# Optimization experiments

Hardware: AMD Instinct MI355X
Metric: run time of the kernel (lower is better)

## Reference

```python
import jax, jax.numpy as jnp
import numpy as np

NEG_BIG = -1e9

def setup_inputs() -> dict:
    key = jax.random.key(0)
    kq, kk, kv, kwq, kwk, kwv, km = jax.random.split(key, 7)
    B, S, d = 16, 1024, 512
    Q = jax.random.normal(kq, (B, S, d), dtype=jnp.float32)
    K = jax.random.normal(kk, (B, S, d), dtype=jnp.float32)
    V = jax.random.normal(kv, (B, S, d), dtype=jnp.float32)
    # nn.Linear weights [d, d]; torch applies x @ W.T
    WQ = jax.random.normal(kwq, (d, d), dtype=jnp.float32) / np.sqrt(d)
    WK = jax.random.normal(kwk, (d, d), dtype=jnp.float32) / np.sqrt(d)
    WV = jax.random.normal(kwv, (d, d), dtype=jnp.float32) / np.sqrt(d)
    mask = jax.random.randint(km, (B, S), 0, 2, dtype=jnp.int32)
    return {"Q": Q, "K": K, "V": V, "WQ": WQ, "WK": WK, "WV": WV, "mask": mask}


def reference(Q, K, V, WQ, WK, WV, mask):
    d = Q.shape[-1]
    q = jnp.einsum('bsd,ed->bse', Q, WQ)
    k = jnp.einsum('bsd,ed->bse', K, WK)
    v = jnp.einsum('bsd,ed->bse', V, WV)
    scores = jnp.einsum('bqd,bkd->bqk', q, k) / jnp.sqrt(jnp.float32(d))
    attn = jax.nn.softmax(scores, axis=-1)
    # Faithful to original: mask applied AFTER softmax with -1e9 fill
    m = mask[:, None, :]  # [B,1,S] broadcast over query dim
    attn = jnp.where(m == 0, jnp.float32(NEG_BIG), attn)
    out = jnp.einsum('bqk,bkd->bqd', attn, v)
    return (out, attn)
```

## Files before the change

kernel.cpp:

```cpp
#include <hip/hip_runtime.h>
#include <hip/hip_bf16.h>

typedef float f32x4 __attribute__((ext_vector_type(4)));
typedef __bf16 bf16x8 __attribute__((ext_vector_type(8)));
typedef unsigned short u16x8 __attribute__((ext_vector_type(8)));
typedef int i32x4 __attribute__((ext_vector_type(4)));

#define NEG_BIG_F (-1000000000.0f)
#define SCALE_F 0.044194173824159216f

__device__ __forceinline__ unsigned short f2bf(float f) {
  unsigned int u = __float_as_uint(f);
  u += 0x7FFFu + ((u >> 16) & 1u);
  return (unsigned short)(u >> 16);
}

__device__ __forceinline__ float bf2f(unsigned short h) {
  return __uint_as_float((unsigned int)h << 16);
}

__device__ __forceinline__ u16x8 cvt8(f32x4 a, f32x4 b) {
  u16x8 r;
  r[0] = f2bf(a[0]); r[1] = f2bf(a[1]); r[2] = f2bf(a[2]); r[3] = f2bf(a[3]);
  r[4] = f2bf(b[0]); r[5] = f2bf(b[1]); r[6] = f2bf(b[2]); r[7] = f2bf(b[3]);
  return r;
}

__device__ __forceinline__ void gload16(const void* g, char* l) {
  __builtin_amdgcn_global_load_lds(
      (const __attribute__((address_space(1))) unsigned int*)g,
      (__attribute__((address_space(3))) unsigned int*)l, 16, 0, 0);
}

__global__ __launch_bounds__(256) void cvtW(
    const float* __restrict__ w0, const float* __restrict__ w1,
    const float* __restrict__ w2, unsigned short* __restrict__ out)
{
  const float* src = blockIdx.z == 0 ? w0 : (blockIdx.z == 1 ? w1 : w2);
  unsigned short* dst = out + (size_t)blockIdx.z * 262144;
  const int i = (blockIdx.x * 256 + threadIdx.x) * 8;
  f32x4 a = *(const f32x4*)(src + i);
  f32x4 b = *(const f32x4*)(src + i + 4);
  *(u16x8*)&dst[i] = cvt8(a, b);
}

__global__ __launch_bounds__(512, 2) void proj_all(
    const float* __restrict__ Q, const float* __restrict__ Kx,
    const float* __restrict__ V, const unsigned short* __restrict__ wb,
    unsigned short* __restrict__ qb, unsigned short* __restrict__ kb,
    unsigned short* __restrict__ vt)
{
  __shared__ __align__(16) unsigned short lds[32768];

  const int bid = blockIdx.x;
  const int tid = threadIdx.x;
  const int lane = tid & 63, wave = tid >> 6;
  const int fr = lane & 15, fq = lane >> 4;

  if (bid < 256) {
    const int z = bid >> 7, rem = bid & 127;
    const float* X = z ? Kx : Q;
    const unsigned short* W = wb + (size_t)z * 262144;
    unsigned short* Y = z ? kb : qb;
    const int m0 = (rem & 63) * 256, n0 = (rem >> 6) * 256;
    const int wr = (wave >> 2) * 128, wc = (wave & 3) * 64;

    unsigned short (*As)[256][32] = (unsigned short (*)[256][32])lds;
    unsigned short (*Bs)[256][32] = (unsigned short (*)[256][32])(lds + 16384);

    f32x4 acc[8][4] = {};

    int arow_s[2], aswz_s[2];
    const float* gAs[2];
    #pragma unroll
    for (int i = 0; i < 2; i++) {
      const int c = tid + 512 * i;
      arow_s[i] = c >> 2;
      aswz_s[i] = ((c & 3) ^ ((arow_s[i] >> 1) & 3)) * 8;
      gAs[i] = X + (size_t)(m0 + arow_s[i]) * 512 + (c & 3) * 8;
    }
    const unsigned short* gB[2]; char* lB[2];
    #pragma unroll
    for (int i = 0; i < 2; i++) {
      const int c = tid + 512 * i, row = c >> 2, slot = c & 3;
      gB[i] = W + (size_t)(n0 + row) * 512 + (slot ^ ((row >> 1) & 3)) * 8;
      lB[i] = (char*)(lds + 16384) + c * 16;
    }

    f32x4 pa[2][2];
    #pragma unroll
    for (int i = 0; i < 2; i++) {
      pa[i][0] = *(const f32x4*)(gAs[i]);
      pa[i][1] = *(const f32x4*)(gAs[i] + 4);
    }
    #pragma unroll
    for (int i = 0; i < 2; i++) gload16(gB[i], lB[i]);
    #pragma unroll
    for (int i = 0; i < 2; i++)
      *(u16x8*)&As[0][arow_s[i]][aswz_s[i]] = cvt8(pa[i][0], pa[i][1]);

    int cur = 0;
    for (int kt = 0; kt < 512; kt += 32) {
      const int nb = cur ^ 1;
      if (kt < 480) {
        #pragma unroll
        for (int i = 0; i < 2; i++) {
          pa[i][0] = *(const f32x4*)(gAs[i] + kt + 32);
          pa[i][1] = *(const f32x4*)(gAs[i] + kt + 36);
        }
        #pragma unroll
        for (int i = 0; i < 2; i++) gload16(gB[i] + kt + 32, lB[i] + nb * 16384);
        asm volatile("s_waitcnt vmcnt(6) lgkmcnt(0)" ::: "memory");
      } else {
        asm volatile("s_waitcnt vmcnt(0) lgkmcnt(0)" ::: "memory");
      }
      __builtin_amdgcn_sched_barrier(0);
      __builtin_amdgcn_s_barrier();

      bf16x8 bv[4];
      #pragma unroll
      for (int nf = 0; nf < 4; nf++) {
        const int br = wc + nf * 16 + fr;
        bv[nf] = *(const bf16x8*)&Bs[cur][br][(fq ^ ((br >> 1) & 3)) * 8];
      }
      #pragma unroll
      for (int mf = 0; mf < 8; mf++) {
        const int ar = wr + mf * 16 + fr;
        bf16x8 av = *(const bf16x8*)&As[cur][ar][(fq ^ ((ar >> 1) & 3)) * 8];
        #pragma unroll
        for (int nf = 0; nf < 4; nf++)
          acc[mf][nf] = __builtin_amdgcn_mfma_f32_16x16x32_bf16(av, bv[nf], acc[mf][nf], 0, 0, 0);
      }

      if (kt < 480) {
        #pragma unroll
        for (int i = 0; i < 2; i++)
          *(u16x8*)&As[nb][arow_s[i]][aswz_s[i]] = cvt8(pa[i][0], pa[i][1]);
      }
      __builtin_amdgcn_s_barrier();
      cur = nb;
    }

    #pragma unroll
    for (int mf = 0; mf < 8; mf++)
      #pragma unroll
      for (int nf = 0; nf < 4; nf++)
        #pragma unroll
        for (int rr = 0; rr < 4; rr++) {
          const int m = m0 + wr + mf * 16 + fq * 4 + rr;
          const int n = n0 + wc + nf * 16 + fr;
          Y[(size_t)m * 512 + n] = f2bf(acc[mf][nf][rr]);
        }
  } else {
    const int c0 = bid - 256;
    const int m0 = (c0 & 3) * 128, n0 = ((c0 >> 2) & 3) * 256, b = c0 >> 4;
    const int wr = (wave >> 2) * 64, wc = (wave & 3) * 64;
    const unsigned short* wv = wb + 524288;

    unsigned short (*As)[128][32] = (unsigned short (*)[128][32])lds;
    unsigned short (*Bs)[256][32] = (unsigned short (*)[256][32])(lds + 8192);

    f32x4 acc[4][4] = {};

    const int ar_s = tid >> 2, aslot = tid & 3;
    const unsigned short* gA = wv + (size_t)(m0 + ar_s) * 512 + (aslot ^ ((ar_s >> 1) & 3)) * 8;
    char* lA = (char*)lds + tid * 16;

    int brow_s[2], bswz_s[2];
    const float* gBs[2];
    #pragma unroll
    for (int i = 0; i < 2; i++) {
      const int c = tid + 512 * i;
      brow_s[i] = c >> 2;
      bswz_s[i] = ((c & 3) ^ ((brow_s[i] >> 1) & 3)) * 8;
      gBs[i] = V + ((size_t)b * 1024 + n0 + brow_s[i]) * 512 + (c & 3) * 8;
    }

    f32x4 pb[2][2];
    #pragma unroll
    for (int i = 0; i < 2; i++) {
      pb[i][0] = *(const f32x4*)(gBs[i]);
      pb[i][1] = *(const f32x4*)(gBs[i] + 4);
    }
    gload16(gA, lA);
    #pragma unroll
    for (int i = 0; i < 2; i++)
      *(u16x8*)&Bs[0][brow_s[i]][bswz_s[i]] = cvt8(pb[i][0], pb[i][1]);

    int cur = 0;
    for (int kt = 0; kt < 512; kt += 32) {
      const int nb = cur ^ 1;
      if (kt < 480) {
        #pragma unroll
        for (int i = 0; i < 2; i++) {
          pb[i][0] = *(const f32x4*)(gBs[i] + kt + 32);
          pb[i][1] = *(const f32x4*)(gBs[i] + kt + 36);
        }
        gload16(gA + kt + 32, lA + nb * 8192);
        asm volatile("s_waitcnt vmcnt(5) lgkmcnt(0)" ::: "memory");
      } else {
        asm volatile("s_waitcnt vmcnt(0) lgkmcnt(0)" ::: "memory");
      }
      __builtin_amdgcn_sched_barrier(0);
      __builtin_amdgcn_s_barrier();

      bf16x8 av[4], bv[4];
      #pragma unroll
      for (int mf = 0; mf < 4; mf++) {
        const int ar = wr + mf * 16 + fr;
        av[mf] = *(const bf16x8*)&As[cur][ar][(fq ^ ((ar >> 1) & 3)) * 8];
      }
      #pragma unroll
      for (int nf = 0; nf < 4; nf++) {
        const int br = wc + nf * 16 + fr;
        bv[nf] = *(const bf16x8*)&Bs[cur][br][(fq ^ ((br >> 1) & 3)) * 8];
      }
      #pragma unroll
      for (int mf = 0; mf < 4; mf++)
        #pragma unroll
        for (int nf = 0; nf < 4; nf++)
          acc[mf][nf] = __builtin_amdgcn_mfma_f32_16x16x32_bf16(av[mf], bv[nf], acc[mf][nf], 0, 0, 0);

      if (kt < 480) {
        #pragma unroll
        for (int i = 0; i < 2; i++)
          *(u16x8*)&Bs[nb][brow_s[i]][bswz_s[i]] = cvt8(pb[i][0], pb[i][1]);
      }
      __builtin_amdgcn_s_barrier();
      cur = nb;
    }

    #pragma unroll
    for (int mf = 0; mf < 4; mf++)
      #pragma unroll
      for (int nf = 0; nf < 4; nf++)
        #pragma unroll
        for (int rr = 0; rr < 4; rr++) {
          const int e = m0 + wr + mf * 16 + fq * 4 + rr;
          const int s = n0 + wc + nf * 16 + fr;
          vt[((size_t)b * 512 + e) * 1024 + s] = f2bf(acc[mf][nf][rr]);
        }
  }
}

__global__ __launch_bounds__(512, 2) void score256(
    const unsigned short* __restrict__ qb, const unsigned short* __restrict__ kb,
    const int* __restrict__ mask,
    unsigned short* __restrict__ P, float* __restrict__ partial)
{
  __shared__ __align__(16) unsigned short As[2][256][32];
  __shared__ __align__(16) unsigned short Bs[2][256][32];

  const int tid = threadIdx.x, bz = blockIdx.z;
  const int m0 = blockIdx.x * 256, n0 = blockIdx.y * 256;
  const int lane = tid & 63, wave = tid >> 6;
  const int wr = (wave >> 2) * 128, wc = (wave & 3) * 64;
  const int fr = lane & 15, fq = lane >> 4;

  f32x4 acc[8][4] = {};

  const unsigned short* gA[2]; char* lA[2];
  const unsigned short* gB[2]; char* lB[2];
  #pragma unroll
  for (int i = 0; i < 2; i++) {
    const int c = tid + 512 * i, row = c >> 2, slot = c & 3;
    const int sw = (slot ^ ((row >> 1) & 3)) * 8;
    gA[i] = qb + ((size_t)bz * 1024 + m0 + row) * 512 + sw;
    gB[i] = kb + ((size_t)bz * 1024 + n0 + row) * 512 + sw;
    lA[i] = (char*)&As[0][0][0] + c * 16;
    lB[i] = (char*)&Bs[0][0][0] + c * 16;
  }

  #pragma unroll
  for (int i = 0; i < 2; i++) { gload16(gA[i], lA[i]); gload16(gB[i], lB[i]); }

  int cur = 0;
  for (int kt = 0; kt < 512; kt += 32) {
    const int nb = cur ^ 1;
    if (kt < 480) {
      #pragma unroll
      for (int i = 0; i < 2; i++) {
        gload16(gA[i] + kt + 32, lA[i] + nb * 16384);
        gload16(gB[i] + kt + 32, lB[i] + nb * 16384);
      }
      asm volatile("s_waitcnt vmcnt(4) lgkmcnt(0)" ::: "memory");
    } else {
      asm volatile("s_waitcnt vmcnt(0) lgkmcnt(0)" ::: "memory");
    }
    __builtin_amdgcn_sched_barrier(0);
    __builtin_amdgcn_s_barrier();

    bf16x8 bv[4];
    #pragma unroll
    for (int nf = 0; nf < 4; nf++) {
      const int br = wc + nf * 16 + fr;
      bv[nf] = *(const bf16x8*)&Bs[cur][br][(fq ^ ((br >> 1) & 3)) * 8];
    }
    #pragma unroll
    for (int mf = 0; mf < 8; mf++) {
      const int ar = wr + mf * 16 + fr;
      bf16x8 av = *(const bf16x8*)&As[cur][ar][(fq ^ ((ar >> 1) & 3)) * 8];
      #pragma unroll
      for (int nf = 0; nf < 4; nf++)
        acc[mf][nf] = __builtin_amdgcn_mfma_f32_16x16x32_bf16(av, bv[nf], acc[mf][nf], 0, 0, 0);
    }
    __builtin_amdgcn_s_barrier();
    cur = nb;
  }

  int mcol[4];
  #pragma unroll
  for (int nf = 0; nf < 4; nf++)
    mcol[nf] = mask[bz * 1024 + n0 + wc + nf * 16 + fr];

  unsigned short* Pb = P + ((size_t)bz << 20);
  const int slot = blockIdx.y * 4 + (wave & 3);
  #pragma unroll
  for (int mf = 0; mf < 8; mf++) {
    #pragma unroll
    for (int rr = 0; rr < 4; rr++) {
      const int m = m0 + wr + mf * 16 + fq * 4 + rr;
      float e = 0.f;
      #pragma unroll
      for (int nf = 0; nf < 4; nf++) {
        const float ev = __expf(acc[mf][nf][rr] * SCALE_F);
        e += ev;
        Pb[(size_t)m * 1024 + n0 + wc + nf * 16 + fr] =
            mcol[nf] ? f2bf(ev) : (unsigned short)0;
      }
      e += __shfl_xor(e, 1); e += __shfl_xor(e, 2);
      e += __shfl_xor(e, 4); e += __shfl_xor(e, 8);
      if (fr == 0)
        partial[(size_t)slot * 16384 + bz * 1024 + m] = e;
    }
  }
}

__global__ __launch_bounds__(256) void mv_attn(
    const unsigned short* __restrict__ vt, const unsigned short* __restrict__ P,
    const float* __restrict__ partial, const int* __restrict__ mask,
    float* __restrict__ mvsum, float* __restrict__ attn)
{
  const int bid = blockIdx.x;
  const int tid = threadIdx.x;
  if (bid < 2048) {
    const int row = bid * 4 + (tid >> 6);
    const int b = row >> 9;
    const int lane = tid & 63;
    const unsigned short* vr = vt + (size_t)row * 1024 + lane * 16;
    const int* mr = mask + b * 1024 + lane * 16;
    u16x8 v0 = *(const u16x8*)(vr);
    u16x8 v1 = *(const u16x8*)(vr + 8);
    float s = 0.f;
    #pragma unroll
    for (int j = 0; j < 8; j++) {
      if (!mr[j])     s += bf2f(v0[j]);
      if (!mr[8 + j]) s += bf2f(v1[j]);
    }
    #pragma unroll
    for (int o = 32; o > 0; o >>= 1) s += __shfl_xor(s, o);
    if (lane == 0) mvsum[row] = s;
  } else {
    const int ab = bid - 2048;
    __shared__ float s_inv[2];
    const int row0 = ab * 2;
    if (tid < 2) {
      float s = 0.f;
      #pragma unroll
      for (int p = 0; p < 16; p++) s += partial[(size_t)p * 16384 + row0 + tid];
      s_inv[tid] = 1.0f / s;
    }
    __syncthreads();
    const size_t base = (size_t)ab * 2048 + tid * 8;
    const int b = (int)(base >> 20);
    const int k0 = (int)(base & 1023);
    const u16x8 p8 = *(const u16x8*)(P + base);
    const float iv = s_inv[tid >> 7];
    const int* mr = mask + b * 1024 + k0;
    const i32x4 ma = *(const i32x4*)(mr);
    const i32x4 mb = *(const i32x4*)(mr + 4);
    f32x4 o0, o1;
    o0[0] = ma[0] ? bf2f(p8[0]) * iv : NEG_BIG_F;
    o0[1] = ma[1] ? bf2f(p8[1]) * iv : NEG_BIG_F;
    o0[2] = ma[2] ? bf2f(p8[2]) * iv : NEG_BIG_F;
    o0[3] = ma[3] ? bf2f(p8[3]) * iv : NEG_BIG_F;
    o1[0] = mb[0] ? bf2f(p8[4]) * iv : NEG_BIG_F;
    o1[1] = mb[1] ? bf2f(p8[5]) * iv : NEG_BIG_F;
    o1[2] = mb[2] ? bf2f(p8[6]) * iv : NEG_BIG_F;
    o1[3] = mb[3] ? bf2f(p8[7]) * iv : NEG_BIG_F;
    *(f32x4*)(attn + base) = o0;
    *(f32x4*)(attn + base + 4) = o1;
  }
}

__global__ __launch_bounds__(512) void pv_gemm(
    const unsigned short* __restrict__ P, const unsigned short* __restrict__ vt,
    const float* __restrict__ partial, const float* __restrict__ mvsum,
    float* __restrict__ out)
{
  __shared__ __align__(16) unsigned short As[2][64][32];
  __shared__ __align__(16) unsigned short Bs[2][512][32];
  __shared__ float inv_l[64];

  const int tid = threadIdx.x;
  const int bz = blockIdx.z, m0 = blockIdx.x * 64;
  const int lane = tid & 63, wave = tid >> 6;
  const int n0 = wave * 64;
  const int fr = lane & 15, fq = lane >> 4;

  f32x4 acc[4][4] = {};

  if (tid < 64) {
    float s = 0.f;
    #pragma unroll
    for (int p = 0; p < 16; p++) s += partial[(size_t)p * 16384 + bz * 1024 + m0 + tid];
    inv_l[tid] = 1.0f / s;
  }

  const unsigned short* gA = nullptr; char* lA = nullptr;
  if (tid < 256) {
    const int row = tid >> 2, slot = tid & 3;
    gA = P + ((size_t)bz << 20) + (size_t)(m0 + row) * 1024 + (slot ^ ((row >> 1) & 3)) * 8;
    lA = (char*)&As[0][0][0] + tid * 16;
  }
  const unsigned short* gB[4]; char* lB[4];
  #pragma unroll
  for (int i = 0; i < 4; i++) {
    const int c = tid + 512 * i, row = c >> 2, slot = c & 3;
    gB[i] = vt + ((size_t)bz * 512 + row) * 1024 + (slot ^ ((row >> 1) & 3)) * 8;
    lB[i] = (char*)&Bs[0][0][0] + c * 16;
  }

  if (tid < 256) gload16(gA, lA);
  #pragma unroll
  for (int i = 0; i < 4; i++) gload16(gB[i], lB[i]);

  int cur = 0;
  for (int t = 0; t < 32; t++) {
    const int nb = cur ^ 1;
    const int kt = t * 32;
    if (t < 31) {
      if (tid < 256) gload16(gA + kt + 32, lA + nb * 4096);
      #pragma unroll
      for (int i = 0; i < 4; i++) gload16(gB[i] + kt + 32, lB[i] + nb * 32768);
      if (wave < 4) asm volatile("s_waitcnt vmcnt(5) lgkmcnt(0)" ::: "memory");
      else          asm volatile("s_waitcnt vmcnt(4) lgkmcnt(0)" ::: "memory");
    } else {
      asm volatile("s_waitcnt vmcnt(0) lgkmcnt(0)" ::: "memory");
    }
    __builtin_amdgcn_sched_barrier(0);
    __builtin_amdgcn_s_barrier();

    bf16x8 af[4], bv[4];
    #pragma unroll
    for (int mf = 0; mf < 4; mf++) {
      const int ar = mf * 16 + fr;
      af[mf] = *(const bf16x8*)&As[cur][ar][(fq ^ ((ar >> 1) & 3)) * 8];
    }
    #pragma unroll
    for (int nf = 0; nf < 4; nf++) {
      const int br = n0 + nf * 16 + fr;
      bv[nf] = *(const bf16x8*)&Bs[cur][br][(fq ^ ((br >> 1) & 3)) * 8];
    }
    #pragma unroll
    for (int mf = 0; mf < 4; mf++)
      #pragma unroll
      for (int nf = 0; nf < 4; nf++)
        acc[mf][nf] = __builtin_amdgcn_mfma_f32_16x16x32_bf16(af[mf], bv[nf], acc[mf][nf], 0, 0, 0);
    __builtin_amdgcn_s_barrier();
    cur = nb;
  }

  float mvv[4];
  #pragma unroll
  for (int nf = 0; nf < 4; nf++)
    mvv[nf] = mvsum[bz * 512 + n0 + nf * 16 + fr];
  #pragma unroll
  for (int mf = 0; mf < 4; mf++)
    #pragma unroll
    for (int rr = 0; rr < 4; rr++) {
      const int m = m0 + mf * 16 + fq * 4 + rr;
      const float iv = inv_l[mf * 16 + fq * 4 + rr];
      #pragma unroll
      for (int nf = 0; nf < 4; nf++)
        out[((size_t)bz * 1024 + m) * 512 + n0 + nf * 16 + fr] =
            iv * acc[mf][nf][rr] + NEG_BIG_F * mvv[nf];
    }
}

extern "C" void kernel_launch(void* const* d_in, const int* in_sizes, int n_in,
                              void* d_out, int out_size, void* d_ws, size_t ws_size,
                              hipStream_t stream)
{
  const float* Q  = (const float*)d_in[0];
  const float* Kx = (const float*)d_in[1];
  const float* V  = (const float*)d_in[2];
  const float* WQ = (const float*)d_in[3];
  const float* WK = (const float*)d_in[4];
  const float* WV = (const float*)d_in[5];
  const int* mask = (const int*)d_in[6];

  const int B = 16, S = 1024, D = 512;
  float* out_f  = (float*)d_out;
  float* attn_f = out_f + (size_t)B * S * D;
  unsigned short* Pbuf = (unsigned short*)d_out;

  unsigned short* qb = (unsigned short*)d_ws;
  unsigned short* kb = qb + (size_t)B * S * D;
  unsigned short* vt = kb + (size_t)B * S * D;
  unsigned short* wb = vt + (size_t)B * S * D;
  float* partial = (float*)(wb + 786432);
  float* mvsum = partial + 262144;

  cvtW<<<dim3(128, 1, 3), 256, 0, stream>>>(WQ, WK, WV, wb);
  proj_all<<<dim3(512), 512, 0, stream>>>(Q, Kx, V, wb, qb, kb, vt);
  score256<<<dim3(4, 4, 16), 512, 0, stream>>>(qb, kb, mask, Pbuf, partial);
  mv_attn<<<dim3(10240), 256, 0, stream>>>(vt, Pbuf, partial, mask, mvsum, attn_f);
  pv_gemm<<<dim3(16, 1, 16), 512, 0, stream>>>(Pbuf, vt, partial, mvsum, out_f);
}
```

Baseline: 149.1 us.

## Prefetch fp32 operand tiles two k-steps ahead in projection GEMMs

The projection kernel now holds fp32 register prefetches two k-tiles deep instead of one, using a double-buffered register array. The k-loop is fully unrolled so the buffer indices and vmcnt wait counts are compile-time constants per iteration. The aim is to hide more global-load latency for the fp32 activation loads that are converted to bf16 before the LDS store. In exchange it uses more VGPRs and more code, which could lower occupancy under the 512-thread launch bound.

```diff
diff --git a/kernel.cpp b/kernel.cpp
--- a/kernel.cpp
+++ b/kernel.cpp
@@ -87,33 +87,41 @@
       lB[i] = (char*)(lds + 16384) + c * 16;
     }
 
-    f32x4 pa[2][2];
+    f32x4 pa[2][2][2];
     #pragma unroll
     for (int i = 0; i < 2; i++) {
-      pa[i][0] = *(const f32x4*)(gAs[i]);
-      pa[i][1] = *(const f32x4*)(gAs[i] + 4);
+      pa[0][i][0] = *(const f32x4*)(gAs[i]);
+      pa[0][i][1] = *(const f32x4*)(gAs[i] + 4);
+      pa[1][i][0] = *(const f32x4*)(gAs[i] + 32);
+      pa[1][i][1] = *(const f32x4*)(gAs[i] + 36);
     }
     #pragma unroll
     for (int i = 0; i < 2; i++) gload16(gB[i], lB[i]);
     #pragma unroll
     for (int i = 0; i < 2; i++)
-      *(u16x8*)&As[0][arow_s[i]][aswz_s[i]] = cvt8(pa[i][0], pa[i][1]);
-
-    int cur = 0;
-    for (int kt = 0; kt < 512; kt += 32) {
-      const int nb = cur ^ 1;
-      if (kt < 480) {
+      *(u16x8*)&As[0][arow_s[i]][aswz_s[i]] = cvt8(pa[0][i][0], pa[0][i][1]);
+
+    #pragma unroll
+    for (int t = 0; t < 16; t++) {
+      const int cur = t & 1, nxt = cur ^ 1;
+      const int kt = t * 32;
+      if (t < 15) {
+        #pragma unroll
+        for (int i = 0; i < 2; i++) gload16(gB[i] + kt + 32, lB[i] + nxt * 16384);
+      }
+      if (t < 14) {
         #pragma unroll
         for (int i = 0; i < 2; i++) {
-          pa[i][0] = *(const f32x4*)(gAs[i] + kt + 32);
-          pa[i][1] = *(const f32x4*)(gAs[i] + kt + 36);
+          pa[cur][i][0] = *(const f32x4*)(gAs[i] + kt + 64);
+          pa[cur][i][1] = *(const f32x4*)(gAs[i] + kt + 68);
         }
-        #pragma unroll
-        for (int i = 0; i < 2; i++) gload16(gB[i] + kt + 32, lB[i] + nb * 16384);
+      }
+      if (t == 0 || t == 14)
         asm volatile("s_waitcnt vmcnt(6) lgkmcnt(0)" ::: "memory");
-      } else {
+      else if (t == 15)
         asm volatile("s_waitcnt vmcnt(0) lgkmcnt(0)" ::: "memory");
-      }
+      else
+        asm volatile("s_waitcnt vmcnt(10) lgkmcnt(0)" ::: "memory");
       __builtin_amdgcn_sched_barrier(0);
       __builtin_amdgcn_s_barrier();
 
@@ -132,13 +140,12 @@
           acc[mf][nf] = __builtin_amdgcn_mfma_f32_16x16x32_bf16(av, bv[nf], acc[mf][nf], 0, 0, 0);
       }
 
-      if (kt < 480) {
+      if (t < 15) {
         #pragma unroll
         for (int i = 0; i < 2; i++)
-          *(u16x8*)&As[nb][arow_s[i]][aswz_s[i]] = cvt8(pa[i][0], pa[i][1]);
+          *(u16x8*)&As[nxt][arow_s[i]][aswz_s[i]] = cvt8(pa[nxt][i][0], pa[nxt][i][1]);
       }
       __builtin_amdgcn_s_barrier();
-      cur = nb;
     }
 
     #pragma unroll
@@ -176,31 +183,37 @@
       gBs[i] = V + ((size_t)b * 1024 + n0 + brow_s[i]) * 512 + (c & 3) * 8;
     }
 
-    f32x4 pb[2][2];
+    f32x4 pb[2][2][2];
     #pragma unroll
     for (int i = 0; i < 2; i++) {
-      pb[i][0] = *(const f32x4*)(gBs[i]);
-      pb[i][1] = *(const f32x4*)(gBs[i] + 4);
+      pb[0][i][0] = *(const f32x4*)(gBs[i]);
+      pb[0][i][1] = *(const f32x4*)(gBs[i] + 4);
+      pb[1][i][0] = *(const f32x4*)(gBs[i] + 32);
+      pb[1][i][1] = *(const f32x4*)(gBs[i] + 36);
     }
     gload16(gA, lA);
     #pragma unroll
     for (int i = 0; i < 2; i++)
-      *(u16x8*)&Bs[0][brow_s[i]][bswz_s[i]] = cvt8(pb[i][0], pb[i][1]);
-
-    int cur = 0;
-    for (int kt = 0; kt < 512; kt += 32) {
-      const int nb = cur ^ 1;
-      if (kt < 480) {
+      *(u16x8*)&Bs[0][brow_s[i]][bswz_s[i]] = cvt8(pb[0][i][0], pb[0][i][1]);
+
+    #pragma unroll
+    for (int t = 0; t < 16; t++) {
+      const int cur = t & 1, nxt = cur ^ 1;
+      const int kt = t * 32;
+      if (t < 15) gload16(gA + kt + 32, lA + nxt * 8192);
+      if (t < 14) {
         #pragma unroll
         for (int i = 0; i < 2; i++) {
-          pb[i][0] = *(const f32x4*)(gBs[i] + kt + 32);
-          pb[i][1] = *(const f32x4*)(gBs[i] + kt + 36);
+          pb[cur][i][0] = *(const f32x4*)(gBs[i] + kt + 64);
+          pb[cur][i][1] = *(const f32x4*)(gBs[i] + kt + 68);
         }
-        gload16(gA + kt + 32, lA + nb * 8192);
+      }
+      if (t == 0 || t == 14)
         asm volatile("s_waitcnt vmcnt(5) lgkmcnt(0)" ::: "memory");
-      } else {
+      else if (t == 15)
         asm volatile("s_waitcnt vmcnt(0) lgkmcnt(0)" ::: "memory");
-      }
+      else
+        asm volatile("s_waitcnt vmcnt(9) lgkmcnt(0)" ::: "memory");
       __builtin_amdgcn_sched_barrier(0);
       __builtin_amdgcn_s_barrier();
 
@@ -221,13 +234,12 @@
         for (int nf = 0; nf < 4; nf++)
           acc[mf][nf] = __builtin_amdgcn_mfma_f32_16x16x32_bf16(av[mf], bv[nf], acc[mf][nf], 0, 0, 0);
 
-      if (kt < 480) {
+      if (t < 15) {
         #pragma unroll
         for (int i = 0; i < 2; i++)
-          *(u16x8*)&Bs[nb][brow_s[i]][bswz_s[i]] = cvt8(pb[i][0], pb[i][1]);
+          *(u16x8*)&Bs[nxt][brow_s[i]][bswz_s[i]] = cvt8(pb[nxt][i][0], pb[nxt][i][1]);
       }
       __builtin_amdgcn_s_barrier();
-      cur = nb;
     }
 
     #pragma unroll
```

After: 147.0 us. No clear change (-1.5%).

## Split projection kernel and stage fp32 activations via async LDS loads

Applied to the files above, without the earlier changes.

Splits the fused projection kernel into separate Q/K and V kernels. The fp32 activation tiles now go straight to LDS through global_load_lds with an XOR swizzle, and are converted to bf16 when fragments are read. This replaces the old path of register prefetch, convert, then LDS store. The Q/K tile shrinks from 256 to 128 rows, giving twice as many blocks. In exchange, LDS traffic roughly doubles for the fp32 operand, conversion work is repeated per wave in the inner loop, and there is an extra kernel launch.

```diff
diff --git a/kernel.cpp b/kernel.cpp
--- a/kernel.cpp
+++ b/kernel.cpp
@@ -24,6 +24,10 @@
   r[0] = f2bf(a[0]); r[1] = f2bf(a[1]); r[2] = f2bf(a[2]); r[3] = f2bf(a[3]);
   r[4] = f2bf(b[0]); r[5] = f2bf(b[1]); r[6] = f2bf(b[2]); r[7] = f2bf(b[3]);
   return r;
+}
+
+__device__ __forceinline__ bf16x8 u2b(u16x8 u) {
+  union { u16x8 u; bf16x8 b; } c; c.u = u; return c.b;
 }
 
 __device__ __forceinline__ void gload16(const void* g, char* l) {
@@ -44,203 +48,172 @@
   *(u16x8*)&dst[i] = cvt8(a, b);
 }
 
-__global__ __launch_bounds__(512, 2) void proj_all(
+__global__ __launch_bounds__(512, 2) void projqk(
     const float* __restrict__ Q, const float* __restrict__ Kx,
-    const float* __restrict__ V, const unsigned short* __restrict__ wb,
-    unsigned short* __restrict__ qb, unsigned short* __restrict__ kb,
-    unsigned short* __restrict__ vt)
-{
-  __shared__ __align__(16) unsigned short lds[32768];
+    const unsigned short* __restrict__ wb,
+    unsigned short* __restrict__ qb, unsigned short* __restrict__ kb)
+{
+  __shared__ __align__(16) float          Af[2][128][32];
+  __shared__ __align__(16) unsigned short Bs[2][256][32];
 
   const int bid = blockIdx.x;
+  const int z = bid >> 8, rem = bid & 255;
+  const float* X = z ? Kx : Q;
+  const unsigned short* W = wb + (size_t)z * 262144;
+  unsigned short* Y = z ? kb : qb;
+  const int m0 = (rem >> 1) * 128, n0 = (rem & 1) * 256;
   const int tid = threadIdx.x;
   const int lane = tid & 63, wave = tid >> 6;
+  const int wr = (wave >> 2) * 64, wc = (wave & 3) * 64;
   const int fr = lane & 15, fq = lane >> 4;
 
-  if (bid < 256) {
-    const int z = bid >> 7, rem = bid & 127;
-    const float* X = z ? Kx : Q;
-    const unsigned short* W = wb + (size_t)z * 262144;
-    unsigned short* Y = z ? kb : qb;
-    const int m0 = (rem & 63) * 256, n0 = (rem >> 6) * 256;
-    const int wr = (wave >> 2) * 128, wc = (wave & 3) * 64;
-
-    unsigned short (*As)[256][32] = (unsigned short (*)[256][32])lds;
-    unsigned short (*Bs)[256][32] = (unsigned short (*)[256][32])(lds + 16384);
-
-    f32x4 acc[8][4] = {};
-
-    int arow_s[2], aswz_s[2];
-    const float* gAs[2];
-    #pragma unroll
-    for (int i = 0; i < 2; i++) {
-      const int c = tid + 512 * i;
-      arow_s[i] = c >> 2;
-      aswz_s[i] = ((c & 3) ^ ((arow_s[i] >> 1) & 3)) * 8;
-      gAs[i] = X + (size_t)(m0 + arow_s[i]) * 512 + (c & 3) * 8;
-    }
-    const unsigned short* gB[2]; char* lB[2];
-    #pragma unroll
-    for (int i = 0; i < 2; i++) {
-      const int c = tid + 512 * i, row = c >> 2, slot = c & 3;
-      gB[i] = W + (size_t)(n0 + row) * 512 + (slot ^ ((row >> 1) & 3)) * 8;
-      lB[i] = (char*)(lds + 16384) + c * 16;
-    }
-
-    f32x4 pa[2][2];
-    #pragma unroll
-    for (int i = 0; i < 2; i++) {
-      pa[i][0] = *(const f32x4*)(gAs[i]);
-      pa[i][1] = *(const f32x4*)(gAs[i] + 4);
-    }
-    #pragma unroll
-    for (int i = 0; i < 2; i++) gload16(gB[i], lB[i]);
-    #pragma unroll
-    for (int i = 0; i < 2; i++)
-      *(u16x8*)&As[0][arow_s[i]][aswz_s[i]] = cvt8(pa[i][0], pa[i][1]);
-
-    int cur = 0;
-    for (int kt = 0; kt < 512; kt += 32) {
-      const int nb = cur ^ 1;
-      if (kt < 480) {
-        #pragma unroll
-        for (int i = 0; i < 2; i++) {
-          pa[i][0] = *(const f32x4*)(gAs[i] + kt + 32);
-          pa[i][1] = *(const f32x4*)(gAs[i] + kt + 36);
-        }
-        #pragma unroll
-        for (int i = 0; i < 2; i++) gload16(gB[i] + kt + 32, lB[i] + nb * 16384);
-        asm volatile("s_waitcnt vmcnt(6) lgkmcnt(0)" ::: "memory");
-      } else {
-        asm volatile("s_waitcnt vmcnt(0) lgkmcnt(0)" ::: "memory");
+  f32x4 acc[4][4] = {};
+
+  const float* gA[2]; char* lA[2];
+  #pragma unroll
+  for (int i = 0; i < 2; i++) {
+    const int c = tid + 512 * i, row = c >> 3, slot = c & 7;
+    gA[i] = X + (size_t)(m0 + row) * 512 + (slot ^ (row & 7)) * 4;
+    lA[i] = (char*)&Af[0][0][0] + c * 16;
+  }
+  const unsigned short* gB[2]; char* lB[2];
+  #pragma unroll
+  for (int i = 0; i < 2; i++) {
+    const int c = tid + 512 * i, row = c >> 2, slot = c & 3;
+    gB[i] = W + (size_t)(n0 + row) * 512 + (slot ^ ((row >> 1) & 3)) * 8;
+    lB[i] = (char*)&Bs[0][0][0] + c * 16;
+  }
+
+  #pragma unroll
+  for (int i = 0; i < 2; i++) { gload16(gA[i], lA[i]); gload16(gB[i], lB[i]); }
+
+  int cur = 0;
+  for (int kt = 0; kt < 512; kt += 32) {
+    const int nb = cur ^ 1;
+    if (kt < 480) {
+      #pragma unroll
+      for (int i = 0; i < 2; i++) {
+        gload16(gA[i] + kt + 32, lA[i] + nb * 16384);
+        gload16(gB[i] + kt + 32, lB[i] + nb * 16384);
       }
-      __builtin_amdgcn_sched_barrier(0);
-      __builtin_amdgcn_s_barrier();
-
-      bf16x8 bv[4];
-      #pragma unroll
-      for (int nf = 0; nf < 4; nf++) {
-        const int br = wc + nf * 16 + fr;
-        bv[nf] = *(const bf16x8*)&Bs[cur][br][(fq ^ ((br >> 1) & 3)) * 8];
+      asm volatile("s_waitcnt vmcnt(4) lgkmcnt(0)" ::: "memory");
+    } else {
+      asm volatile("s_waitcnt vmcnt(0) lgkmcnt(0)" ::: "memory");
+    }
+    __builtin_amdgcn_sched_barrier(0);
+    __builtin_amdgcn_s_barrier();
+
+    bf16x8 av[4], bv[4];
+    #pragma unroll
+    for (int nf = 0; nf < 4; nf++) {
+      const int br = wc + nf * 16 + fr;
+      bv[nf] = *(const bf16x8*)&Bs[cur][br][(fq ^ ((br >> 1) & 3)) * 8];
+    }
+    #pragma unroll
+    for (int mf = 0; mf < 4; mf++) {
+      const int ar = wr + mf * 16 + fr;
+      f32x4 lo = *(const f32x4*)&Af[cur][ar][((fq * 2)     ^ (ar & 7)) * 4];
+      f32x4 hi = *(const f32x4*)&Af[cur][ar][((fq * 2 + 1) ^ (ar & 7)) * 4];
+      av[mf] = u2b(cvt8(lo, hi));
+    }
+    #pragma unroll
+    for (int mf = 0; mf < 4; mf++)
+      #pragma unroll
+      for (int nf = 0; nf < 4; nf++)
+        acc[mf][nf] = __builtin_amdgcn_mfma_f32_16x16x32_bf16(av[mf], bv[nf], acc[mf][nf], 0, 0, 0);
+    __builtin_amdgcn_s_barrier();
+    cur = nb;
+  }
+
+  #pragma unroll
+  for (int mf = 0; mf < 4; mf++)
+    #pragma unroll
+    for (int nf = 0; nf < 4; nf++)
+      #pragma unroll
+      for (int rr = 0; rr < 4; rr++) {
+        const int m = m0 + wr + mf * 16 + fq * 4 + rr;
+        const int n = n0 + wc + nf * 16 + fr;
+        Y[(size_t)m * 512 + n] = f2bf(acc[mf][nf][rr]);
       }
-      #pragma unroll
-      for (int mf = 0; mf < 8; mf++) {
-        const int ar = wr + mf * 16 + fr;
-        bf16x8 av = *(const bf16x8*)&As[cur][ar][(fq ^ ((ar >> 1) & 3)) * 8];
-        #pragma unroll
-        for (int nf = 0; nf < 4; nf++)
-          acc[mf][nf] = __builtin_amdgcn_mfma_f32_16x16x32_bf16(av, bv[nf], acc[mf][nf], 0, 0, 0);
+}
+
+__global__ __launch_bounds__(512, 2) void projv(
+    const float* __restrict__ V, const unsigned short* __restrict__ wv,
+    unsigned short* __restrict__ vt)
+{
+  __shared__ __align__(16) unsigned short As[2][128][32];
+  __shared__ __align__(16) float          Bf[2][256][32];
+
+  const int bid = blockIdx.x;
+  const int m0 = (bid & 3) * 128, n0 = ((bid >> 2) & 3) * 256, b = bid >> 4;
+  const int tid = threadIdx.x;
+  const int lane = tid & 63, wave = tid >> 6;
+  const int wr = (wave >> 2) * 64, wc = (wave & 3) * 64;
+  const int fr = lane & 15, fq = lane >> 4;
+
+  f32x4 acc[4][4] = {};
+
+  const int arw = tid >> 2, asl = tid & 3;
+  const unsigned short* gA = wv + (size_t)(m0 + arw) * 512 + (asl ^ ((arw >> 1) & 3)) * 8;
+  char* lA = (char*)&As[0][0][0] + tid * 16;
+  const float* gB[4]; char* lB[4];
+  #pragma unroll
+  for (int i = 0; i < 4; i++) {
+    const int c = tid + 512 * i, row = c >> 3, slot = c & 7;
+    gB[i] = V + ((size_t)b * 1024 + n0 + row) * 512 + (slot ^ (row & 7)) * 4;
+    lB[i] = (char*)&Bf[0][0][0] + c * 16;
+  }
+
+  gload16(gA, lA);
+  #pragma unroll
+  for (int i = 0; i < 4; i++) gload16(gB[i], lB[i]);
+
+  int cur = 0;
+  for (int kt = 0; kt < 512; kt += 32) {
+    const int nb = cur ^ 1;
+    if (kt < 480) {
+      gload16(gA + kt + 32, lA + nb * 8192);
+      #pragma unroll
+      for (int i = 0; i < 4; i++) gload16(gB[i] + kt + 32, lB[i] + nb * 32768);
+      asm volatile("s_waitcnt vmcnt(5) lgkmcnt(0)" ::: "memory");
+    } else {
+      asm volatile("s_waitcnt vmcnt(0) lgkmcnt(0)" ::: "memory");
+    }
+    __builtin_amdgcn_sched_barrier(0);
+    __builtin_amdgcn_s_barrier();
+
+    bf16x8 av[4], bv[4];
+    #pragma unroll
+    for (int mf = 0; mf < 4; mf++) {
+      const int ar = wr + mf * 16 + fr;
+      av[mf] = *(const bf16x8*)&As[cur][ar][(fq ^ ((ar >> 1) & 3)) * 8];
+    }
+    #pragma unroll
+    for (int nf = 0; nf < 4; nf++) {
+      const int br = wc + nf * 16 + fr;
+      f32x4 lo = *(const f32x4*)&Bf[cur][br][((fq * 2)     ^ (br & 7)) * 4];
+      f32x4 hi = *(const f32x4*)&Bf[cur][br][((fq * 2 + 1) ^ (br & 7)) * 4];
+      bv[nf] = u2b(cvt8(lo, hi));
+    }
+    #pragma unroll
+    for (int mf = 0; mf < 4; mf++)
+      #pragma unroll
+      for (int nf = 0; nf < 4; nf++)
+        acc[mf][nf] = __builtin_amdgcn_mfma_f32_16x16x32_bf16(av[mf], bv[nf], acc[mf][nf], 0, 0, 0);
+    __builtin_amdgcn_s_barrier();
+    cur = nb;
+  }
+
+  #pragma unroll
+  for (int mf = 0; mf < 4; mf++)
+    #pragma unroll
+    for (int nf = 0; nf < 4; nf++)
+      #pragma unroll
+      for (int rr = 0; rr < 4; rr++) {
+        const int e = m0 + wr + mf * 16 + fq * 4 + rr;
+        const int s = n0 + wc + nf * 16 + fr;
+        vt[((size_t)b * 512 + e) * 1024 + s] = f2bf(acc[mf][nf][rr]);
       }
-
-      if (kt < 480) {
-        #pragma unroll
-        for (int i = 0; i < 2; i++)
-          *(u16x8*)&As[nb][arow_s[i]][aswz_s[i]] = cvt8(pa[i][0], pa[i][1]);
-      }
-      __builtin_amdgcn_s_barrier();
-      cur = nb;
-    }
-
-    #pragma unroll
-    for (int mf = 0; mf < 8; mf++)
-      #pragma unroll
-      for (int nf = 0; nf < 4; nf++)
-        #pragma unroll
-        for (int rr = 0; rr < 4; rr++) {
-          const int m = m0 + wr + mf * 16 + fq * 4 + rr;
-          const int n = n0 + wc + nf * 16 + fr;
-          Y[(size_t)m * 512 + n] = f2bf(acc[mf][nf][rr]);
-        }
-  } else {
-    const int c0 = bid - 256;
-    const int m0 = (c0 & 3) * 128, n0 = ((c0 >> 2) & 3) * 256, b = c0 >> 4;
-    const int wr = (wave >> 2) * 64, wc = (wave & 3) * 64;
-    const unsigned short* wv = wb + 524288;
-
-    unsigned short (*As)[128][32] = (unsigned short (*)[128][32])lds;
-    unsigned short (*Bs)[256][32] = (unsigned short (*)[256][32])(lds + 8192);
-
-    f32x4 acc[4][4] = {};
-
-    const int ar_s = tid >> 2, aslot = tid & 3;
-    const unsigned short* gA = wv + (size_t)(m0 + ar_s) * 512 + (aslot ^ ((ar_s >> 1) & 3)) * 8;
-    char* lA = (char*)lds + tid * 16;
-
-    int brow_s[2], bswz_s[2];
-    const float* gBs[2];
-    #pragma unroll
-    for (int i = 0; i < 2; i++) {
-      const int c = tid + 512 * i;
-      brow_s[i] = c >> 2;
-      bswz_s[i] = ((c & 3) ^ ((brow_s[i] >> 1) & 3)) * 8;
-      gBs[i] = V + ((size_t)b * 1024 + n0 + brow_s[i]) * 512 + (c & 3) * 8;
-    }
-
-    f32x4 pb[2][2];
-    #pragma unroll
-    for (int i = 0; i < 2; i++) {
-      pb[i][0] = *(const f32x4*)(gBs[i]);
-      pb[i][1] = *(const f32x4*)(gBs[i] + 4);
-    }
-    gload16(gA, lA);
-    #pragma unroll
-    for (int i = 0; i < 2; i++)
-      *(u16x8*)&Bs[0][brow_s[i]][bswz_s[i]] = cvt8(pb[i][0], pb[i][1]);
-
-    int cur = 0;
-    for (int kt = 0; kt < 512; kt += 32) {
-      const int nb = cur ^ 1;
-      if (kt < 480) {
-        #pragma unroll
-        for (int i = 0; i < 2; i++) {
-          pb[i][0] = *(const f32x4*)(gBs[i] + kt + 32);
-          pb[i][1] = *(const f32x4*)(gBs[i] + kt + 36);
-        }
-        gload16(gA + kt + 32, lA + nb * 8192);
-        asm volatile("s_waitcnt vmcnt(5) lgkmcnt(0)" ::: "memory");
-      } else {
-        asm volatile("s_waitcnt vmcnt(0) lgkmcnt(0)" ::: "memory");
-      }
-      __builtin_amdgcn_sched_barrier(0);
-      __builtin_amdgcn_s_barrier();
-
-      bf16x8 av[4], bv[4];
-      #pragma unroll
-      for (int mf = 0; mf < 4; mf++) {
-        const int ar = wr + mf * 16 + fr;
-        av[mf] = *(const bf16x8*)&As[cur][ar][(fq ^ ((ar >> 1) & 3)) * 8];
-      }
-      #pragma unroll
-      for (int nf = 0; nf < 4; nf++) {
-        const int br = wc + nf * 16 + fr;
-        bv[nf] = *(const bf16x8*)&Bs[cur][br][(fq ^ ((br >> 1) & 3)) * 8];
-      }
-      #pragma unroll
-      for (int mf = 0; mf < 4; mf++)
-        #pragma unroll
-        for (int nf = 0; nf < 4; nf++)
-          acc[mf][nf] = __builtin_amdgcn_mfma_f32_16x16x32_bf16(av[mf], bv[nf], acc[mf][nf], 0, 0, 0);
-
-      if (kt < 480) {
-        #pragma unroll
-        for (int i = 0; i < 2; i++)
-          *(u16x8*)&Bs[nb][brow_s[i]][bswz_s[i]] = cvt8(pb[i][0], pb[i][1]);
-      }
-      __builtin_amdgcn_s_barrier();
-      cur = nb;
-    }
-
-    #pragma unroll
-    for (int mf = 0; mf < 4; mf++)
-      #pragma unroll
-      for (int nf = 0; nf < 4; nf++)
-        #pragma unroll
-        for (int rr = 0; rr < 4; rr++) {
-          const int e = m0 + wr + mf * 16 + fq * 4 + rr;
-          const int s = n0 + wc + nf * 16 + fr;
-          vt[((size_t)b * 512 + e) * 1024 + s] = f2bf(acc[mf][nf][rr]);
-        }
-  }
 }
 
 __global__ __launch_bounds__(512, 2) void score256(
@@ -513,7 +486,8 @@
   float* mvsum = partial + 262144;
 
   cvtW<<<dim3(128, 1, 3), 256, 0, stream>>>(WQ, WK, WV, wb);
-  proj_all<<<dim3(512), 512, 0, stream>>>(Q, Kx, V, wb, qb, kb, vt);
+  projqk<<<dim3(512), 512, 0, stream>>>(Q, Kx, wb, qb, kb);
+  projv<<<dim3(256), 512, 0, stream>>>(V, wb + 524288, vt);
   score256<<<dim3(4, 4, 16), 512, 0, stream>>>(qb, kb, mask, Pbuf, partial);
   mv_attn<<<dim3(10240), 256, 0, stream>>>(vt, Pbuf, partial, mask, mvsum, attn_f);
   pv_gemm<<<dim3(16, 1, 16), 512, 0, stream>>>(Pbuf, vt, partial, mvsum, out_f);
```

New measurement: 155.1 us. +4.0%, slower.
